# Optimization experiments

Hardware: AMD Instinct MI355X
Metric: run time of the kernel (lower is better)

## Reference

```python
import jax, jax.numpy as jnp
import numpy as np

ALPHA = 2.0
INF = 1e12  # stand-in for +inf, safe in fp32 arithmetic here


def _sq_dt_last(f):
    """Generalized 1D squared distance transform along the last axis.
    D[..., p] = min_q (p - q)^2 + f[..., q]  (Felzenszwalb DT, brute-force min)."""
    n = f.shape[-1]
    i = jnp.arange(n, dtype=f.dtype)
    cost = (i[:, None] - i[None, :]) ** 2  # [q, p]
    # [..., q, 1] + [q, p] -> min over q
    return jnp.min(f[..., :, None] + cost, axis=-2)


def _edt(mask):
    """Exact 2D Euclidean distance transform: distance from each True pixel
    to the nearest False pixel (0 at False pixels), matching scipy's
    distance_transform_edt(mask). mask: bool [B, H, W]."""
    f = jnp.where(mask, jnp.float32(INF), jnp.float32(0.0))
    # pass along H (axis 1)
    f = jnp.moveaxis(_sq_dt_last(jnp.moveaxis(f, 1, -1)), -1, 1)
    # pass along W (axis 2)
    f = _sq_dt_last(f)
    return jnp.sqrt(f)


def _distance_field(img):
    """fg_dist + bg_dist per batch element; zero field if no foreground
    (mirrors the fg_mask.any() check in the torch code)."""
    fg = img > 0.5
    field = _edt(fg) + _edt(~fg)
    has_fg = jnp.any(fg, axis=(1, 2), keepdims=True)
    return jnp.where(has_fg, field, jnp.float32(0.0))


def setup_inputs() -> dict:
    key = jax.random.key(0)
    k1, k2 = jax.random.split(key)
    pred = jax.random.normal(k1, (8, 192, 192), dtype=jnp.float32)   # logits
    target = jax.random.uniform(k2, (8, 192, 192), dtype=jnp.float32)
    return {"pred": pred, "target": target}


def reference(pred, target):
    p = jax.nn.sigmoid(pred)
    # distance fields are computed via numpy/scipy in the original -> constants
    pred_dt = jax.lax.stop_gradient(_distance_field(p))
    target_dt = jax.lax.stop_gradient(_distance_field(target))
    pred_error = (p - target) ** 2
    distance = (pred_dt ** ALPHA + target_dt ** ALPHA) / (pred_dt + target_dt) ** ALPHA
    dt_field = pred_error * distance
    loss = jnp.mean(dt_field, axis=-1)
    return jnp.mean(loss)
```

## Files before the change

kernel.cpp:

```cpp
#include <hip/hip_runtime.h>
#include <stdint.h>

#define B 8
#define H 192
#define W 192
#define NPIX (B * H * W)
#define NROWS (B * H)
#define INFF 1e12f

__device__ __forceinline__ int hi_pos(uint64_t w0, uint64_t w1, uint64_t w2) {
  if (w2) return 191 - __builtin_clzll(w2);
  if (w1) return 127 - __builtin_clzll(w1);
  if (w0) return 63 - __builtin_clzll(w0);
  return -255;
}
__device__ __forceinline__ int lo_pos(uint64_t w0, uint64_t w1, uint64_t w2) {
  if (w0) return __builtin_ctzll(w0);
  if (w1) return 64 + __builtin_ctzll(w1);
  if (w2) return 128 + __builtin_ctzll(w2);
  return 447;
}
__device__ __forceinline__ int nearest_dist(uint64_t s0, uint64_t s1,
                                            uint64_t s2, int h) {
  int k = h >> 6, r = h & 63;
  uint64_t keepL = (2ull << r) - 1;
  uint64_t b0 = s0, b1 = s1, b2 = s2;
  if (k == 0) { b0 &= keepL; b1 = 0; b2 = 0; }
  else if (k == 1) { b1 &= keepL; b2 = 0; }
  else { b2 &= keepL; }
  int dbelow = h - hi_pos(b0, b1, b2);
  uint64_t keepU = (~0ull) << r;
  uint64_t a0 = s0, a1 = s1, a2 = s2;
  if (k == 0) { a0 &= keepU; }
  else if (k == 1) { a0 = 0; a1 &= keepU; }
  else { a0 = 0; a1 = 0; a2 &= keepU; }
  int dabove = lo_pos(a0, a1, a2) - h;
  return min(min(dbelow, dabove), 255);
}

__global__ __launch_bounds__(192) void col_pass(
    const float* __restrict__ pred, const float* __restrict__ targ,
    uint32_t* __restrict__ g32) {
  int bw = blockIdx.x;
  int b = bw / W, w = bw % W;
  int h = threadIdx.x;
  __shared__ uint64_t mP[3], mT[3];
  int idx = b * H * W + h * W + w;
  float xv = pred[idx];
  float tv = targ[idx];
  uint64_t bp = __ballot(xv > 0.0f);
  uint64_t bt = __ballot(tv > 0.5f);
  if ((h & 63) == 0) { mP[h >> 6] = bp; mT[h >> 6] = bt; }
  __syncthreads();
  uint64_t p0 = mP[0], p1 = mP[1], p2 = mP[2];
  uint64_t t0 = mT[0], t1 = mT[1], t2 = mT[2];
  int dFp = nearest_dist(~p0, ~p1, ~p2, h);
  int dTp = nearest_dist(p0, p1, p2, h);
  int dFt = nearest_dist(~t0, ~t1, ~t2, h);
  int dTt = nearest_dist(t0, t1, t2, h);
  g32[idx] = (uint32_t)dFp | ((uint32_t)dTp << 8) | ((uint32_t)dFt << 16) |
             ((uint32_t)dTt << 24);
}

__global__ __launch_bounds__(192) void row_pass(
    const float* __restrict__ pred, const float* __restrict__ targ,
    const uint32_t* __restrict__ g32, float* __restrict__ partial) {
  int bh = blockIdx.x;
  int b = bh / H, h = bh % H;
  int w = threadIdx.x;
  __shared__ uint32_t sm[W];
  __shared__ float wsum[3];
  int base = b * H * W + h * W;
  uint32_t own = g32[base + w];
  sm[w] = own;
  float xv = pred[base + w];
  float tv = targ[base + w];
  __syncthreads();

  int shp = (xv > 0.0f) ? 0 : 8;
  int sht = (tv > 0.5f) ? 16 : 24;
  int dp = (own >> shp) & 255;
  int dt = (own >> sht) & 255;
  float bp = (dp == 255) ? INFF : (float)(dp * dp);
  float bt = (dt == 255) ? INFF : (float)(dt * dt);
  for (int r = 1; r < W; ++r) {
    float rr = (float)(r * r);
    if (rr >= fmaxf(bp, bt)) break;
    int ql = w - r, qr = w + r;
    if (ql >= 0) {
      uint32_t v = sm[ql];
      int a = (v >> shp) & 255, c = (v >> sht) & 255;
      bp = fminf(bp, (a == 255) ? INFF : rr + (float)(a * a));
      bt = fminf(bt, (c == 255) ? INFF : rr + (float)(c * c));
    }
    if (qr < W) {
      uint32_t v = sm[qr];
      int a = (v >> shp) & 255, c = (v >> sht) & 255;
      bp = fminf(bp, (a == 255) ? INFF : rr + (float)(a * a));
      bt = fminf(bt, (c == 255) ? INFF : rr + (float)(c * c));
    }
  }

  float p = 1.0f / (1.0f + __expf(-xv));
  float e = p - tv;
  float err = e * e;
  float pd = sqrtf(bp), td = sqrtf(bt);
  float s = pd + td;
  float term = err * (bp + bt) / (s * s);

  for (int off = 32; off > 0; off >>= 1) term += __shfl_down(term, off, 64);
  if ((w & 63) == 0) wsum[w >> 6] = term;
  __syncthreads();
  if (w == 0) partial[bh] = wsum[0] + wsum[1] + wsum[2];
}

__global__ __launch_bounds__(256) void reduce_pass(
    const float* __restrict__ partial, float* __restrict__ out) {
  int t = threadIdx.x;
  float s = 0.0f;
#pragma unroll
  for (int i = t; i < NROWS; i += 256) s += partial[i];
  for (int off = 32; off > 0; off >>= 1) s += __shfl_down(s, off, 64);
  __shared__ float ws[4];
  if ((t & 63) == 0) ws[t >> 6] = s;
  __syncthreads();
  if (t == 0) out[0] = (ws[0] + ws[1] + ws[2] + ws[3]) * (1.0f / (float)NPIX);
}

extern "C" void kernel_launch(void* const* d_in, const int* in_sizes, int n_in,
                              void* d_out, int out_size, void* d_ws, size_t ws_size,
                              hipStream_t stream) {
  const float* pred = (const float*)d_in[0];
  const float* targ = (const float*)d_in[1];
  float* out = (float*)d_out;
  uint32_t* g32 = (uint32_t*)d_ws;
  float* partial = (float*)((char*)d_ws + (size_t)NPIX * 4);

  col_pass<<<B * W, 192, 0, stream>>>(pred, targ, g32);
  row_pass<<<NROWS, 192, 0, stream>>>(pred, targ, g32, partial);
  reduce_pass<<<1, 256, 0, stream>>>(partial, out);
}
```

Measured before the change: 66.93 us.

## Fuse column and row EDT passes into one kernel with an LDS-resident tile

Merges the two distance-transform kernels into one. Each block takes one batch image and a 48-column strip: it builds row bitmasks from float4 loads, computes the row-direction nearest distances into shared memory, then runs the column-direction envelope search and the loss in the same block. This removes the global intermediate buffer and one launch, and shrinks the final reduction to 32 partials. The cost is only 32 blocks, so most of the GPU sits idle and each thread works serially through 24 pixels with data-dependent inner loops.

```diff
diff --git a/kernel.cpp b/kernel.cpp
--- a/kernel.cpp
+++ b/kernel.cpp
@@ -1,12 +1,15 @@
 #include <hip/hip_runtime.h>
 #include <stdint.h>
 
-#define B 8
+#define NB 8
 #define H 192
 #define W 192
-#define NPIX (B * H * W)
-#define NROWS (B * H)
+#define NPIX (NB * H * W)
 #define INFF 1e12f
+#define NBLK 32
+#define TPB 384
+#define CWT 24
+#define GSTRIDE 49
 
 __device__ __forceinline__ int hi_pos(uint64_t w0, uint64_t w1, uint64_t w2) {
   if (w2) return 191 - __builtin_clzll(w2);
@@ -21,110 +24,145 @@
   return 447;
 }
 __device__ __forceinline__ int nearest_dist(uint64_t s0, uint64_t s1,
-                                            uint64_t s2, int h) {
-  int k = h >> 6, r = h & 63;
+                                            uint64_t s2, int p) {
+  int k = p >> 6, r = p & 63;
   uint64_t keepL = (2ull << r) - 1;
   uint64_t b0 = s0, b1 = s1, b2 = s2;
   if (k == 0) { b0 &= keepL; b1 = 0; b2 = 0; }
   else if (k == 1) { b1 &= keepL; b2 = 0; }
   else { b2 &= keepL; }
-  int dbelow = h - hi_pos(b0, b1, b2);
+  int dbelow = p - hi_pos(b0, b1, b2);
   uint64_t keepU = (~0ull) << r;
   uint64_t a0 = s0, a1 = s1, a2 = s2;
   if (k == 0) { a0 &= keepU; }
   else if (k == 1) { a0 = 0; a1 &= keepU; }
   else { a0 = 0; a1 = 0; a2 &= keepU; }
-  int dabove = lo_pos(a0, a1, a2) - h;
+  int dabove = lo_pos(a0, a1, a2) - p;
   return min(min(dbelow, dabove), 255);
 }
 
-__global__ __launch_bounds__(192) void col_pass(
-    const float* __restrict__ pred, const float* __restrict__ targ,
-    uint32_t* __restrict__ g32) {
-  int bw = blockIdx.x;
-  int b = bw / W, w = bw % W;
-  int h = threadIdx.x;
-  __shared__ uint64_t mP[3], mT[3];
-  int idx = b * H * W + h * W + w;
-  float xv = pred[idx];
-  float tv = targ[idx];
-  uint64_t bp = __ballot(xv > 0.0f);
-  uint64_t bt = __ballot(tv > 0.5f);
-  if ((h & 63) == 0) { mP[h >> 6] = bp; mT[h >> 6] = bt; }
-  __syncthreads();
-  uint64_t p0 = mP[0], p1 = mP[1], p2 = mP[2];
-  uint64_t t0 = mT[0], t1 = mT[1], t2 = mT[2];
-  int dFp = nearest_dist(~p0, ~p1, ~p2, h);
-  int dTp = nearest_dist(p0, p1, p2, h);
-  int dFt = nearest_dist(~t0, ~t1, ~t2, h);
-  int dTt = nearest_dist(t0, t1, t2, h);
-  g32[idx] = (uint32_t)dFp | ((uint32_t)dTp << 8) | ((uint32_t)dFt << 16) |
-             ((uint32_t)dTt << 24);
+__device__ __forceinline__ uint64_t shfl_xor_u64(uint64_t x, int m) {
+  uint32_t lo = (uint32_t)x, hi = (uint32_t)(x >> 32);
+  lo = __shfl_xor(lo, m, 64);
+  hi = __shfl_xor(hi, m, 64);
+  return ((uint64_t)hi << 32) | lo;
 }
 
-__global__ __launch_bounds__(192) void row_pass(
+__global__ __launch_bounds__(TPB) void fused(
     const float* __restrict__ pred, const float* __restrict__ targ,
-    const uint32_t* __restrict__ g32, float* __restrict__ partial) {
-  int bh = blockIdx.x;
-  int b = bh / H, h = bh % H;
-  int w = threadIdx.x;
-  __shared__ uint32_t sm[W];
-  __shared__ float wsum[3];
-  int base = b * H * W + h * W;
-  uint32_t own = g32[base + w];
-  sm[w] = own;
-  float xv = pred[base + w];
-  float tv = targ[base + w];
+    float* __restrict__ partial) {
+  int blk = blockIdx.x;
+  int b = blk >> 2;
+  int w0 = (blk & 3) * 48;
+  int t = threadIdx.x;
+  int r = t >> 1;
+  int hf = t & 1;
+  __shared__ uint32_t g[H * GSTRIDE];
+  __shared__ float wsum[TPB / 64];
+
+  const float* prow = pred + b * H * W + r * W + 96 * hf;
+  const float* trow = targ + b * H * W + r * W + 96 * hf;
+  uint64_t pl0 = 0, pl1 = 0, ql0 = 0, ql1 = 0;
+#pragma unroll
+  for (int i = 0; i < 96; i += 4) {
+    float4 pv = *(const float4*)(prow + i);
+    float4 tv = *(const float4*)(trow + i);
+    uint64_t pb = (uint64_t)((int)(pv.x > 0.f) | ((int)(pv.y > 0.f) << 1) |
+                             ((int)(pv.z > 0.f) << 2) | ((int)(pv.w > 0.f) << 3));
+    uint64_t qb = (uint64_t)((int)(tv.x > .5f) | ((int)(tv.y > .5f) << 1) |
+                             ((int)(tv.z > .5f) << 2) | ((int)(tv.w > .5f) << 3));
+    if (i < 64) { pl0 |= pb << i; ql0 |= qb << i; }
+    else        { pl1 |= pb << (i - 64); ql1 |= qb << (i - 64); }
+  }
+  uint64_t pm0 = shfl_xor_u64(pl0, 1), pm1 = shfl_xor_u64(pl1, 1);
+  uint64_t qm0 = shfl_xor_u64(ql0, 1), qm1 = shfl_xor_u64(ql1, 1);
+  uint64_t lo0 = hf ? pm0 : pl0, lo1 = hf ? pm1 : pl1;
+  uint64_t hi0 = hf ? pl0 : pm0, hi1 = hf ? pl1 : pm1;
+  uint64_t p0 = lo0;
+  uint64_t p1 = (lo1 & 0xffffffffull) | (hi0 << 32);
+  uint64_t p2 = (hi0 >> 32) | ((hi1 & 0xffffffffull) << 32);
+  lo0 = hf ? qm0 : ql0; lo1 = hf ? qm1 : ql1;
+  hi0 = hf ? ql0 : qm0; hi1 = hf ? ql1 : qm1;
+  uint64_t q0 = lo0;
+  uint64_t q1 = (lo1 & 0xffffffffull) | (hi0 << 32);
+  uint64_t q2 = (hi0 >> 32) | ((hi1 & 0xffffffffull) << 32);
+
+  int wl0 = CWT * hf;
+#pragma unroll 4
+  for (int i = 0; i < CWT; ++i) {
+    int wl = wl0 + i;
+    int w = w0 + wl;
+    int k = w >> 6, rb = w & 63;
+    uint64_t pw = (k == 0) ? p0 : ((k == 1) ? p1 : p2);
+    uint64_t qw = (k == 0) ? q0 : ((k == 1) ? q1 : q2);
+    int mp = (int)((pw >> rb) & 1);
+    int mt = (int)((qw >> rb) & 1);
+    uint64_t s0 = mp ? ~p0 : p0, s1 = mp ? ~p1 : p1, s2 = mp ? ~p2 : p2;
+    int sp = nearest_dist(s0, s1, s2, w);
+    uint64_t u0 = mt ? ~q0 : q0, u1 = mt ? ~q1 : q1, u2 = mt ? ~q2 : q2;
+    int st = nearest_dist(u0, u1, u2, w);
+    int dFp = mp ? sp : 0, dTp = mp ? 0 : sp;
+    int dFt = mt ? st : 0, dTt = mt ? 0 : st;
+    g[r * GSTRIDE + wl] = (uint32_t)dFp | ((uint32_t)dTp << 8) |
+                          ((uint32_t)dFt << 16) | ((uint32_t)dTt << 24);
+  }
   __syncthreads();
 
-  int shp = (xv > 0.0f) ? 0 : 8;
-  int sht = (tv > 0.5f) ? 16 : 24;
-  int dp = (own >> shp) & 255;
-  int dt = (own >> sht) & 255;
-  float bp = (dp == 255) ? INFF : (float)(dp * dp);
-  float bt = (dt == 255) ? INFF : (float)(dt * dt);
-  for (int r = 1; r < W; ++r) {
-    float rr = (float)(r * r);
-    if (rr >= fmaxf(bp, bt)) break;
-    int ql = w - r, qr = w + r;
-    if (ql >= 0) {
-      uint32_t v = sm[ql];
-      int a = (v >> shp) & 255, c = (v >> sht) & 255;
-      bp = fminf(bp, (a == 255) ? INFF : rr + (float)(a * a));
-      bt = fminf(bt, (c == 255) ? INFF : rr + (float)(c * c));
+  float acc = 0.0f;
+  const float* prow2 = pred + b * H * W + r * W + w0 + wl0;
+  const float* trow2 = targ + b * H * W + r * W + w0 + wl0;
+  for (int i = 0; i < CWT; ++i) {
+    int wl = wl0 + i;
+    float xv = prow2[i];
+    float tv = trow2[i];
+    int shp = (xv > 0.0f) ? 0 : 8;
+    int sht = (tv > 0.5f) ? 16 : 24;
+    uint32_t own = g[r * GSTRIDE + wl];
+    int dp = (own >> shp) & 255;
+    int dt = (own >> sht) & 255;
+    float bp = (dp == 255) ? INFF : (float)(dp * dp);
+    float bt = (dt == 255) ? INFF : (float)(dt * dt);
+    for (int dr = 1; dr < H; ++dr) {
+      float rr = (float)(dr * dr);
+      if (rr >= fmaxf(bp, bt)) break;
+      int ru = r - dr, rd = r + dr;
+      if (ru >= 0) {
+        uint32_t v = g[ru * GSTRIDE + wl];
+        int a = (v >> shp) & 255, c = (v >> sht) & 255;
+        bp = fminf(bp, (a == 255) ? INFF : rr + (float)(a * a));
+        bt = fminf(bt, (c == 255) ? INFF : rr + (float)(c * c));
+      }
+      if (rd < H) {
+        uint32_t v = g[rd * GSTRIDE + wl];
+        int a = (v >> shp) & 255, c = (v >> sht) & 255;
+        bp = fminf(bp, (a == 255) ? INFF : rr + (float)(a * a));
+        bt = fminf(bt, (c == 255) ? INFF : rr + (float)(c * c));
+      }
     }
-    if (qr < W) {
-      uint32_t v = sm[qr];
-      int a = (v >> shp) & 255, c = (v >> sht) & 255;
-      bp = fminf(bp, (a == 255) ? INFF : rr + (float)(a * a));
-      bt = fminf(bt, (c == 255) ? INFF : rr + (float)(c * c));
-    }
+    float p = 1.0f / (1.0f + __expf(-xv));
+    float e = p - tv;
+    float pd = sqrtf(bp), td = sqrtf(bt);
+    float s = pd + td;
+    acc += e * e * (bp + bt) / (s * s);
   }
 
-  float p = 1.0f / (1.0f + __expf(-xv));
-  float e = p - tv;
-  float err = e * e;
-  float pd = sqrtf(bp), td = sqrtf(bt);
-  float s = pd + td;
-  float term = err * (bp + bt) / (s * s);
-
-  for (int off = 32; off > 0; off >>= 1) term += __shfl_down(term, off, 64);
-  if ((w & 63) == 0) wsum[w >> 6] = term;
+  for (int off = 32; off > 0; off >>= 1) acc += __shfl_down(acc, off, 64);
+  if ((t & 63) == 0) wsum[t >> 6] = acc;
   __syncthreads();
-  if (w == 0) partial[bh] = wsum[0] + wsum[1] + wsum[2];
+  if (t == 0) {
+    float s = 0.0f;
+#pragma unroll
+    for (int j = 0; j < TPB / 64; ++j) s += wsum[j];
+    partial[blk] = s;
+  }
 }
 
-__global__ __launch_bounds__(256) void reduce_pass(
+__global__ __launch_bounds__(64) void reduce_pass(
     const float* __restrict__ partial, float* __restrict__ out) {
   int t = threadIdx.x;
-  float s = 0.0f;
-#pragma unroll
-  for (int i = t; i < NROWS; i += 256) s += partial[i];
+  float s = (t < NBLK) ? partial[t] : 0.0f;
   for (int off = 32; off > 0; off >>= 1) s += __shfl_down(s, off, 64);
-  __shared__ float ws[4];
-  if ((t & 63) == 0) ws[t >> 6] = s;
-  __syncthreads();
-  if (t == 0) out[0] = (ws[0] + ws[1] + ws[2] + ws[3]) * (1.0f / (float)NPIX);
+  if (t == 0) out[0] = s * (1.0f / (float)NPIX);
 }
 
 extern "C" void kernel_launch(void* const* d_in, const int* in_sizes, int n_in,
@@ -133,10 +171,8 @@
   const float* pred = (const float*)d_in[0];
   const float* targ = (const float*)d_in[1];
   float* out = (float*)d_out;
-  uint32_t* g32 = (uint32_t*)d_ws;
-  float* partial = (float*)((char*)d_ws + (size_t)NPIX * 4);
+  float* partial = (float*)d_ws;
 
-  col_pass<<<B * W, 192, 0, stream>>>(pred, targ, g32);
-  row_pass<<<NROWS, 192, 0, stream>>>(pred, targ, g32, partial);
-  reduce_pass<<<1, 256, 0, stream>>>(partial, out);
+  fused<<<NBLK, TPB, 0, stream>>>(pred, targ, partial);
+  reduce_pass<<<1, 64, 0, stream>>>(partial, out);
 }
```

Measured after the change: 100.8 us. 50.6% more time.

## Store column bitmasks instead of packed per-pixel column distances

Applied to the files above, without the earlier changes.

The column pass now writes only the 64-bit ballot masks per column, six words per column, instead of a packed 32-bit distance for every pixel. The row pass reloads those masks and recomputes the column nearest distance for its own pixel, choosing the complement based on the pixel's own bit. This removes the full-image intermediate write and read in exchange for some redundant bit arithmetic in the row pass. The column kernel also drops its shared memory and sync.

```diff
diff --git a/kernel.cpp b/kernel.cpp
--- a/kernel.cpp
+++ b/kernel.cpp
@@ -6,6 +6,7 @@
 #define W 192
 #define NPIX (B * H * W)
 #define NROWS (B * H)
+#define NCOL (B * W)
 #define INFF 1e12f
 
 __device__ __forceinline__ int hi_pos(uint64_t w0, uint64_t w1, uint64_t w2) {
@@ -38,43 +39,51 @@
   return min(min(dbelow, dabove), 255);
 }
 
-__global__ __launch_bounds__(192) void col_pass(
+__global__ __launch_bounds__(192) void col_mask(
     const float* __restrict__ pred, const float* __restrict__ targ,
-    uint32_t* __restrict__ g32) {
+    uint64_t* __restrict__ masks) {
   int bw = blockIdx.x;
   int b = bw / W, w = bw % W;
   int h = threadIdx.x;
-  __shared__ uint64_t mP[3], mT[3];
   int idx = b * H * W + h * W + w;
-  float xv = pred[idx];
-  float tv = targ[idx];
-  uint64_t bp = __ballot(xv > 0.0f);
-  uint64_t bt = __ballot(tv > 0.5f);
-  if ((h & 63) == 0) { mP[h >> 6] = bp; mT[h >> 6] = bt; }
-  __syncthreads();
-  uint64_t p0 = mP[0], p1 = mP[1], p2 = mP[2];
-  uint64_t t0 = mT[0], t1 = mT[1], t2 = mT[2];
-  int dFp = nearest_dist(~p0, ~p1, ~p2, h);
-  int dTp = nearest_dist(p0, p1, p2, h);
-  int dFt = nearest_dist(~t0, ~t1, ~t2, h);
-  int dTt = nearest_dist(t0, t1, t2, h);
-  g32[idx] = (uint32_t)dFp | ((uint32_t)dTp << 8) | ((uint32_t)dFt << 16) |
-             ((uint32_t)dTt << 24);
+  uint64_t bp = __ballot(pred[idx] > 0.0f);
+  uint64_t bt = __ballot(targ[idx] > 0.5f);
+  if ((h & 63) == 0) {
+    int wv = h >> 6;
+    masks[wv * NCOL + bw] = bp;
+    masks[(3 + wv) * NCOL + bw] = bt;
+  }
 }
 
 __global__ __launch_bounds__(192) void row_pass(
     const float* __restrict__ pred, const float* __restrict__ targ,
-    const uint32_t* __restrict__ g32, float* __restrict__ partial) {
+    const uint64_t* __restrict__ masks, float* __restrict__ partial) {
   int bh = blockIdx.x;
   int b = bh / H, h = bh % H;
   int w = threadIdx.x;
   __shared__ uint32_t sm[W];
   __shared__ float wsum[3];
+  int cw = b * W + w;
+  uint64_t p0 = masks[0 * NCOL + cw], p1 = masks[1 * NCOL + cw],
+           p2 = masks[2 * NCOL + cw];
+  uint64_t q0 = masks[3 * NCOL + cw], q1 = masks[4 * NCOL + cw],
+           q2 = masks[5 * NCOL + cw];
   int base = b * H * W + h * W;
-  uint32_t own = g32[base + w];
-  sm[w] = own;
   float xv = pred[base + w];
   float tv = targ[base + w];
+
+  int k = h >> 6, rb = h & 63;
+  uint64_t pw = (k == 0) ? p0 : ((k == 1) ? p1 : p2);
+  uint64_t qw = (k == 0) ? q0 : ((k == 1) ? q1 : q2);
+  int mp = (int)((pw >> rb) & 1);
+  int mt = (int)((qw >> rb) & 1);
+  int sp = nearest_dist(mp ? ~p0 : p0, mp ? ~p1 : p1, mp ? ~p2 : p2, h);
+  int st = nearest_dist(mt ? ~q0 : q0, mt ? ~q1 : q1, mt ? ~q2 : q2, h);
+  int dFp = mp ? sp : 0, dTp = mp ? 0 : sp;
+  int dFt = mt ? st : 0, dTt = mt ? 0 : st;
+  uint32_t own = (uint32_t)dFp | ((uint32_t)dTp << 8) | ((uint32_t)dFt << 16) |
+                 ((uint32_t)dTt << 24);
+  sm[w] = own;
   __syncthreads();
 
   int shp = (xv > 0.0f) ? 0 : 8;
@@ -133,10 +142,10 @@
   const float* pred = (const float*)d_in[0];
   const float* targ = (const float*)d_in[1];
   float* out = (float*)d_out;
-  uint32_t* g32 = (uint32_t*)d_ws;
-  float* partial = (float*)((char*)d_ws + (size_t)NPIX * 4);
+  uint64_t* masks = (uint64_t*)d_ws;
+  float* partial = (float*)((char*)d_ws + (size_t)6 * NCOL * 8);
 
-  col_pass<<<B * W, 192, 0, stream>>>(pred, targ, g32);
-  row_pass<<<NROWS, 192, 0, stream>>>(pred, targ, g32, partial);
+  col_mask<<<NCOL, 192, 0, stream>>>(pred, targ, masks);
+  row_pass<<<NROWS, 192, 0, stream>>>(pred, targ, masks, partial);
   reduce_pass<<<1, 256, 0, stream>>>(partial, out);
 }
```

Result: faster. 65.40 us (-2.3%).
